# Optimization experiments

Measured on AMD Instinct MI355X. Metric: run time of the kernel, lower is better.

## Reference

```python
import jax, jax.numpy as jnp
import numpy as np

B, N, H, D = 8, 2048, 8, 64  # batch, seq, heads, head_dim
DM = H * D                   # model dim = 512


def setup_inputs() -> dict:
    key = jax.random.key(0)
    ks = jax.random.split(key, 9)
    std = 0.02
    return {
        "x": jax.random.normal(ks[0], (B, N, DM), dtype=jnp.float32),
        "Wq": jax.random.normal(ks[1], (H, D, D), dtype=jnp.float32) * std,
        "bq": jnp.zeros((H, D), dtype=jnp.float32),
        "Wk": jax.random.normal(ks[2], (H, D, D), dtype=jnp.float32) * std,
        "bk": jnp.zeros((H, D), dtype=jnp.float32),
        "Wv": jax.random.normal(ks[3], (H, D, D), dtype=jnp.float32) * std,
        "bv": jnp.zeros((H, D), dtype=jnp.float32),
        "Wp": jax.random.normal(ks[4], (DM, DM), dtype=jnp.float32) * std,
        "bp": jnp.zeros((DM,), dtype=jnp.float32),
    }


def reference(x, Wq, bq, Wk, bk, Wv, bv, Wp, bp):
    b, n, dm = x.shape
    # rearrange 'b n (h d) -> b h n d'
    xh = x.reshape(b, n, H, D).transpose(0, 2, 1, 3)  # [b,h,n,d]
    # per-head linear projections (torch Linear: y = x W^T + b), batched over heads
    q = jnp.einsum('bhnd,hed->bhne', xh, Wq) + bq[None, :, None, :]
    k = jnp.einsum('bhnd,hed->bhne', xh, Wk) + bk[None, :, None, :]
    v = jnp.einsum('bhnd,hed->bhne', xh, Wv) + bv[None, :, None, :]
    scale = 1.0 / jnp.sqrt(jnp.asarray(D, dtype=x.dtype))
    scores = jnp.einsum('bhqe,bhke->bhqk', q, k) * scale  # [b,h,n,n]
    attn = jax.nn.softmax(scores, axis=-1)
    out = jnp.einsum('bhqk,bhke->bhqe', attn, v)          # [b,h,n,d]
    # 'b h n d -> b n (h d)' then output projection
    out = out.transpose(0, 2, 1, 3).reshape(b, n, H * D)
    return out @ Wp.T + bp
```

## Files before the change

### kernel.cpp

```cpp
#include <hip/hip_runtime.h>
#include <hip/hip_bf16.h>

#define B_ 8
#define N_ 2048
#define H_ 8
#define DM_ 512
#define NT_ 32

typedef __bf16 bf16x8 __attribute__((ext_vector_type(8)));
typedef float f32x4 __attribute__((ext_vector_type(4)));
typedef float f32x16 __attribute__((ext_vector_type(16)));
typedef unsigned short us8 __attribute__((ext_vector_type(8)));
typedef unsigned short us4 __attribute__((ext_vector_type(4)));
typedef unsigned int u32x4 __attribute__((ext_vector_type(4)));

#define QSCALE 0.1803368801111204f

__device__ __forceinline__ int swz(int row, int byte_in_row) {
  return row * 128 + (byte_in_row ^ ((row & 7) << 4));
}

__device__ __forceinline__ unsigned short f2bf(float x) {
  __bf16 h = (__bf16)x;
  return __builtin_bit_cast(unsigned short, h);
}

__device__ __forceinline__ float fexp2(float x) {
#if __has_builtin(__builtin_amdgcn_exp2f)
  return __builtin_amdgcn_exp2f(x);
#else
  return exp2f(x);
#endif
}

__device__ __forceinline__ unsigned cvtpk(float a, float b) {
  unsigned r;
  asm("v_cvt_pk_bf16_f32 %0, %1, %2" : "=v"(r) : "v"(a), "v"(b));
  return r;
}

__device__ __forceinline__ f32x4 mfma16(bf16x8 a, bf16x8 b, f32x4 c) {
  return __builtin_amdgcn_mfma_f32_16x16x32_bf16(a, b, c, 0, 0, 0);
}
__device__ __forceinline__ f32x16 mfma32(bf16x8 a, bf16x8 b, f32x16 c) {
  return __builtin_amdgcn_mfma_f32_32x32x16_bf16(a, b, c, 0, 0, 0);
}

__device__ __forceinline__ bf16x8 ldg8(const unsigned short* p) {
  return *reinterpret_cast<const bf16x8*>(p);
}

__device__ __forceinline__ void stage_f32_tile(const float* __restrict__ src,
                                               int src_stride, char* dst, int t) {
#pragma unroll
  for (int rep = 0; rep < 4; ++rep) {
    int cid = rep * 256 + t;
    int row = cid >> 4, c4 = cid & 15;
    float4 v = *reinterpret_cast<const float4*>(src + (size_t)row * src_stride + c4 * 4);
    us4 o;
    o[0] = f2bf(v.x); o[1] = f2bf(v.y); o[2] = f2bf(v.z); o[3] = f2bf(v.w);
    *reinterpret_cast<us4*>(dst + row * 128 + ((c4 * 8) ^ ((row & 7) << 4))) = o;
  }
}

__device__ __forceinline__ void stage_bf16_tile(const unsigned short* __restrict__ src,
                                                int src_stride, char* dst, int t) {
#pragma unroll
  for (int rep = 0; rep < 2; ++rep) {
    int cid = rep * 256 + t;
    int row = cid >> 3, c = cid & 7;
    us8 v = *reinterpret_cast<const us8*>(src + (size_t)row * src_stride + c * 8);
    *reinterpret_cast<us8*>(dst + row * 128 + ((c * 16) ^ ((row & 7) << 4))) = v;
  }
}

__global__ __launch_bounds__(256, 4) void qkv_kernel(
    const float* __restrict__ x,
    const float* __restrict__ Wq, const float* __restrict__ bq,
    const float* __restrict__ Wk, const float* __restrict__ bk,
    const float* __restrict__ Wv, const float* __restrict__ bv,
    unsigned short* __restrict__ Qf, unsigned short* __restrict__ Kf,
    unsigned short* __restrict__ Vf) {
  __shared__ __align__(16) char sX[8192];
  __shared__ __align__(16) char sWq[8192];
  __shared__ __align__(16) char sWk[8192];
  __shared__ __align__(16) char sWv[8192];

  const int t = threadIdx.x;
  const int bh = blockIdx.y, h = bh & 7, b = bh >> 3;
  const int n0 = blockIdx.x * 64;
  const int lane = t & 63, w = t >> 6, g = lane >> 4, li = lane & 15;

  stage_f32_tile(x + ((size_t)(b * N_ + n0)) * DM_ + h * 64, DM_, sX, t);
  stage_f32_tile(Wq + (size_t)h * 4096, 64, sWq, t);
  stage_f32_tile(Wk + (size_t)h * 4096, 64, sWk, t);
  stage_f32_tile(Wv + (size_t)h * 4096, 64, sWv, t);
  __syncthreads();

  bf16x8 xa0 = *reinterpret_cast<const bf16x8*>(sX + swz(16 * w + li, 16 * g));
  bf16x8 xa1 = *reinterpret_cast<const bf16x8*>(sX + swz(16 * w + li, 64 + 16 * g));

  const size_t seg = (size_t)N_ * 64;
  const int qkbase =
      ((n0 >> 5) + (w >> 1)) * 2048 + (li >> 3) * 256 + (w & 1) * 128 + (li & 7);
  const int vbase =
      (n0 >> 6) * 4096 + w * 512 + (g >> 1) * 256 + 4 * (g & 1) + li * 8;

  unsigned short* Qs = Qf + (size_t)bh * seg;
  unsigned short* Ks = Kf + (size_t)bh * seg;
  unsigned short* Vs = Vf + (size_t)bh * seg;

#pragma unroll
  for (int c = 0; c < 4; ++c) {
    f32x4 a = {0.f, 0.f, 0.f, 0.f};
    bf16x8 b0 = *reinterpret_cast<const bf16x8*>(sWq + swz(c * 16 + li, 16 * g));
    bf16x8 b1 = *reinterpret_cast<const bf16x8*>(sWq + swz(c * 16 + li, 64 + 16 * g));
    a = mfma16(xa0, b0, a);
    a = mfma16(xa1, b1, a);
    float bb = bq[h * 64 + c * 16 + li];
#pragma unroll
    for (int i = 0; i < 4; ++i)
      Qs[qkbase + c * 512 + (4 * g + i) * 8] = f2bf((a[i] + bb) * QSCALE);
  }
#pragma unroll
  for (int c = 0; c < 4; ++c) {
    f32x4 a = {0.f, 0.f, 0.f, 0.f};
    bf16x8 b0 = *reinterpret_cast<const bf16x8*>(sWk + swz(c * 16 + li, 16 * g));
    bf16x8 b1 = *reinterpret_cast<const bf16x8*>(sWk + swz(c * 16 + li, 64 + 16 * g));
    a = mfma16(xa0, b0, a);
    a = mfma16(xa1, b1, a);
    float bb = bk[h * 64 + c * 16 + li];
#pragma unroll
    for (int i = 0; i < 4; ++i)
      Ks[qkbase + c * 512 + (4 * g + i) * 8] = f2bf(a[i] + bb);
  }
#pragma unroll
  for (int c = 0; c < 4; ++c) {
    f32x4 a = {0.f, 0.f, 0.f, 0.f};
    bf16x8 b0 = *reinterpret_cast<const bf16x8*>(sWv + swz(c * 16 + li, 16 * g));
    bf16x8 b1 = *reinterpret_cast<const bf16x8*>(sWv + swz(c * 16 + li, 64 + 16 * g));
    a = mfma16(xa0, b0, a);
    a = mfma16(xa1, b1, a);
    float bb = bv[h * 64 + c * 16 + li];
    us4 pk;
#pragma unroll
    for (int i = 0; i < 4; ++i) pk[i] = f2bf(a[i] + bb);
    *reinterpret_cast<us4*>(Vs + vbase + (c >> 1) * 2048 + (c & 1) * 128) = pk;
  }
}

__global__ __launch_bounds__(256, 3) void attn_kernel(
    const unsigned short* __restrict__ Qf, const unsigned short* __restrict__ Kf,
    const unsigned short* __restrict__ Vf, unsigned short* __restrict__ AOw) {
  const int t = threadIdx.x;
  const int lane = t & 63, w = t >> 6;
  const int lo = lane & 31, hi = lane >> 5;
  const bool hb = hi != 0;

  const int bid = blockIdx.x;
  const int work = (bid & 7) * 128 + (bid >> 3);
  const int bh = work >> 4;
  const int qb = (work & 15) * 4 + w;
  const int h = bh & 7, b = bh >> 3;

  const size_t seg = (size_t)N_ * 64;
  const unsigned short* qp = Qf + (size_t)bh * seg + qb * 2048 + lane * 8;
  const unsigned short* kp = Kf + (size_t)bh * seg + lane * 8;
  const unsigned short* vp = Vf + (size_t)bh * seg + lane * 8;

  bf16x8 qf[4];
#pragma unroll
  for (int dd = 0; dd < 4; ++dd) qf[dd] = ldg8(qp + dd * 512);

  f32x16 o0 = {}, o1 = {};
  float m = -__builtin_inff(), l = 0.f;

#pragma unroll 1
  for (int kt = 0; kt < NT_; ++kt) {
    const unsigned short* kpt = kp + kt * 4096;
    const unsigned short* vpt = vp + kt * 4096;
    bf16x8 kf0[4], kf1[4], vf0[4], vf1[4];
#pragma unroll
    for (int dd = 0; dd < 4; ++dd) {
      kf0[dd] = ldg8(kpt + dd * 512);
      kf1[dd] = ldg8(kpt + 2048 + dd * 512);
    }
#pragma unroll
    for (int ks = 0; ks < 4; ++ks) {
      vf0[ks] = ldg8(vpt + ks * 512);
      vf1[ks] = ldg8(vpt + 2048 + ks * 512);
    }

    f32x16 s0 = {}, s1 = {};
    __builtin_amdgcn_s_setprio(1);
#pragma unroll
    for (int dd = 0; dd < 4; ++dd) {
      s0 = mfma32(kf0[dd], qf[dd], s0);
      s1 = mfma32(kf1[dd], qf[dd], s1);
    }
    __builtin_amdgcn_s_setprio(0);

    float pm;
    {
      float a0 = fmaxf(s0[0], s0[1]), a1 = fmaxf(s0[2], s0[3]);
      float a2 = fmaxf(s0[4], s0[5]), a3 = fmaxf(s0[6], s0[7]);
      float a4 = fmaxf(s0[8], s0[9]), a5 = fmaxf(s0[10], s0[11]);
      float a6 = fmaxf(s0[12], s0[13]), a7 = fmaxf(s0[14], s0[15]);
      float b0 = fmaxf(s1[0], s1[1]), b1 = fmaxf(s1[2], s1[3]);
      float b2 = fmaxf(s1[4], s1[5]), b3 = fmaxf(s1[6], s1[7]);
      float b4 = fmaxf(s1[8], s1[9]), b5 = fmaxf(s1[10], s1[11]);
      float b6 = fmaxf(s1[12], s1[13]), b7 = fmaxf(s1[14], s1[15]);
      a0 = fmaxf(fmaxf(a0, a1), fmaxf(a2, a3));
      a4 = fmaxf(fmaxf(a4, a5), fmaxf(a6, a7));
      b0 = fmaxf(fmaxf(b0, b1), fmaxf(b2, b3));
      b4 = fmaxf(fmaxf(b4, b5), fmaxf(b6, b7));
      pm = fmaxf(fmaxf(a0, a4), fmaxf(b0, b4));
    }
    pm = fmaxf(pm, __shfl_xor(pm, 32));

    if (!__all(pm <= m + 8.0f)) {
      float mn = fmaxf(m, pm);
      float al = fexp2(m - mn);
      l *= al;
#pragma unroll
      for (int r = 0; r < 16; ++r) { o0[r] *= al; o1[r] *= al; }
      m = mn;
    }

    float ts0 = 0.f, ts1 = 0.f, ts2 = 0.f, ts3 = 0.f;
#pragma unroll
    for (int r = 0; r < 16; r += 4) {
      s0[r + 0] = fexp2(s0[r + 0] - m); ts0 += s0[r + 0];
      s0[r + 1] = fexp2(s0[r + 1] - m); ts1 += s0[r + 1];
      s0[r + 2] = fexp2(s0[r + 2] - m); ts2 += s0[r + 2];
      s0[r + 3] = fexp2(s0[r + 3] - m); ts3 += s0[r + 3];
      s1[r + 0] = fexp2(s1[r + 0] - m); ts0 += s1[r + 0];
      s1[r + 1] = fexp2(s1[r + 1] - m); ts1 += s1[r + 1];
      s1[r + 2] = fexp2(s1[r + 2] - m); ts2 += s1[r + 2];
      s1[r + 3] = fexp2(s1[r + 3] - m); ts3 += s1[r + 3];
    }
    float ts = (ts0 + ts1) + (ts2 + ts3);
    ts += __shfl_xor(ts, 32);
    l += ts;

    unsigned pl0[4], ph0[4], pl1[4], ph1[4];
#pragma unroll
    for (int qi = 0; qi < 4; ++qi) {
      pl0[qi] = cvtpk(s0[4 * qi + 0], s0[4 * qi + 1]);
      ph0[qi] = cvtpk(s0[4 * qi + 2], s0[4 * qi + 3]);
      pl1[qi] = cvtpk(s1[4 * qi + 0], s1[4 * qi + 1]);
      ph1[qi] = cvtpk(s1[4 * qi + 2], s1[4 * qi + 3]);
    }
    bf16x8 pf[4];
#pragma unroll
    for (int ks = 0; ks < 4; ++ks) {
      const int p = ks & 1;
      unsigned k0l, k0h, k1l, k1h;
      if (ks < 2) { k0l = pl0[2 * p]; k0h = ph0[2 * p]; k1l = pl0[2 * p + 1]; k1h = ph0[2 * p + 1]; }
      else        { k0l = pl1[2 * p]; k0h = ph1[2 * p]; k1l = pl1[2 * p + 1]; k1h = ph1[2 * p + 1]; }
      unsigned sl = hb ? k0l : k1l, sh = hb ? k0h : k1h;
      unsigned rl = __shfl_xor(sl, 32), rh = __shfl_xor(sh, 32);
      unsigned Al = hb ? rl : k0l, Ah = hb ? rh : k0h;
      unsigned Bl = hb ? k1l : rl, Bh = hb ? k1h : rh;
      u32x4 words = {Al, Ah, Bl, Bh};
      pf[ks] = __builtin_bit_cast(bf16x8, words);
    }

    __builtin_amdgcn_s_setprio(1);
#pragma unroll
    for (int ks = 0; ks < 4; ++ks) {
      o0 = mfma32(vf0[ks], pf[ks], o0);
      o1 = mfma32(vf1[ks], pf[ks], o1);
    }
    __builtin_amdgcn_s_setprio(0);
  }

  const float invl = 1.0f / l;
  unsigned short* aoptr =
      AOw + ((size_t)(b * N_) + qb * 32 + lo) * DM_ + h * 64 + 4 * hi;
#pragma unroll
  for (int qi = 0; qi < 4; ++qi) {
    us4 pk;
#pragma unroll
    for (int rr = 0; rr < 4; ++rr) pk[rr] = f2bf(o0[4 * qi + rr] * invl);
    *reinterpret_cast<us4*>(aoptr + 8 * qi) = pk;
  }
#pragma unroll
  for (int qi = 0; qi < 4; ++qi) {
    us4 pk;
#pragma unroll
    for (int rr = 0; rr < 4; ++rr) pk[rr] = f2bf(o1[4 * qi + rr] * invl);
    *reinterpret_cast<us4*>(aoptr + 32 + 8 * qi) = pk;
  }
}

__global__ __launch_bounds__(256, 4) void proj_kernel(
    const unsigned short* __restrict__ AOw, const float* __restrict__ Wp,
    const float* __restrict__ bp, float* __restrict__ out) {
  __shared__ __align__(16) char sA[8192];
  __shared__ __align__(16) char sB[8192];

  const int t = threadIdx.x;
  const int r0 = blockIdx.x * 64;
  const int i0 = blockIdx.y * 64;
  const int lane = t & 63, w = t >> 6, g = lane >> 4, li = lane & 15;

  f32x4 acc[4];
#pragma unroll
  for (int c = 0; c < 4; ++c) {
    acc[c][0] = 0.f; acc[c][1] = 0.f; acc[c][2] = 0.f; acc[c][3] = 0.f;
  }

  for (int jt = 0; jt < 8; ++jt) {
    __syncthreads();
    stage_bf16_tile(AOw + (size_t)r0 * DM_ + jt * 64, DM_, sA, t);
    stage_f32_tile(Wp + (size_t)i0 * DM_ + jt * 64, DM_, sB, t);
    __syncthreads();

    bf16x8 a0 = *reinterpret_cast<const bf16x8*>(sA + swz(16 * w + li, 16 * g));
    bf16x8 a1 = *reinterpret_cast<const bf16x8*>(sA + swz(16 * w + li, 64 + 16 * g));
#pragma unroll
    for (int c = 0; c < 4; ++c) {
      bf16x8 b0 = *reinterpret_cast<const bf16x8*>(sB + swz(c * 16 + li, 16 * g));
      bf16x8 b1 = *reinterpret_cast<const bf16x8*>(sB + swz(c * 16 + li, 64 + 16 * g));
      acc[c] = mfma16(a0, b0, acc[c]);
      acc[c] = mfma16(a1, b1, acc[c]);
    }
  }

#pragma unroll
  for (int c = 0; c < 4; ++c) {
    float bb = bp[i0 + c * 16 + li];
#pragma unroll
    for (int i = 0; i < 4; ++i)
      out[(size_t)(r0 + 16 * w + 4 * g + i) * DM_ + i0 + c * 16 + li] = acc[c][i] + bb;
  }
}

extern "C" void kernel_launch(void* const* d_in, const int* in_sizes, int n_in,
                              void* d_out, int out_size, void* d_ws, size_t ws_size,
                              hipStream_t stream) {
  const float* x  = (const float*)d_in[0];
  const float* Wq = (const float*)d_in[1];
  const float* bq = (const float*)d_in[2];
  const float* Wk = (const float*)d_in[3];
  const float* bk = (const float*)d_in[4];
  const float* Wv = (const float*)d_in[5];
  const float* bv = (const float*)d_in[6];
  const float* Wp = (const float*)d_in[7];
  const float* bp = (const float*)d_in[8];
  float* out = (float*)d_out;

  const size_t seg = (size_t)B_ * H_ * N_ * 64;
  unsigned short* Qf  = (unsigned short*)d_ws;
  unsigned short* Kf  = Qf + seg;
  unsigned short* Vf  = Kf + seg;
  unsigned short* AOw = Vf + seg;

  qkv_kernel<<<dim3(32, 64), 256, 0, stream>>>(x, Wq, bq, Wk, bk, Wv, bv, Qf, Kf, Vf);
  attn_kernel<<<dim3(1024), 256, 0, stream>>>(Qf, Kf, Vf, AOw);
  proj_kernel<<<dim3(256, 8), 256, 0, stream>>>(AOw, Wp, bp, out);
}
```

Measured before the change: 148.4 us.

## Prefetch next K tile, fold max subtraction into MFMA init, use permlane32 swap

The attention inner loop is unrolled by two with ping-pong K register buffers, so the next tile's K fragments load while the current tile computes. The running max is subtracted by seeding the score accumulators with -m, which drops the per-element subtraction before exp2. The shfl_xor plus select sequence that exchanges P halves across lanes is replaced with v_permlane32_swap. The double K buffer adds register pressure, which could hurt occupancy under launch_bounds(256,3).

```diff
diff --git a/kernel.cpp b/kernel.cpp
--- a/kernel.cpp
+++ b/kernel.cpp
@@ -37,6 +37,16 @@
   unsigned r;
   asm("v_cvt_pk_bf16_f32 %0, %1, %2" : "=v"(r) : "v"(a), "v"(b));
   return r;
+}
+
+__device__ __forceinline__ void plswap(unsigned& a, unsigned& b) {
+#if __has_builtin(__builtin_amdgcn_permlane32_swap)
+  auto r = __builtin_amdgcn_permlane32_swap(a, b, false, false);
+  a = r[0];
+  b = r[1];
+#else
+  asm("v_permlane32_swap_b32 %0, %1" : "+v"(a), "+v"(b));
+#endif
 }
 
 __device__ __forceinline__ f32x4 mfma16(bf16x8 a, bf16x8 b, f32x4 c) {
@@ -154,8 +164,7 @@
     const unsigned short* __restrict__ Vf, unsigned short* __restrict__ AOw) {
   const int t = threadIdx.x;
   const int lane = t & 63, w = t >> 6;
-  const int lo = lane & 31, hi = lane >> 5;
-  const bool hb = hi != 0;
+  const int lo = lane & 31;
 
   const int bid = blockIdx.x;
   const int work = (bid & 7) * 128 + (bid >> 3);
@@ -172,31 +181,34 @@
 #pragma unroll
   for (int dd = 0; dd < 4; ++dd) qf[dd] = ldg8(qp + dd * 512);
 
+  bf16x8 kA[8], kB[8];
+#pragma unroll
+  for (int j = 0; j < 8; ++j) kA[j] = ldg8(kp + j * 512);
+
   f32x16 o0 = {}, o1 = {};
-  float m = -__builtin_inff(), l = 0.f;
-
-#pragma unroll 1
-  for (int kt = 0; kt < NT_; ++kt) {
-    const unsigned short* kpt = kp + kt * 4096;
-    const unsigned short* vpt = vp + kt * 4096;
-    bf16x8 kf0[4], kf1[4], vf0[4], vf1[4];
+  float m = 0.f, l = 0.f;
+
+  auto TILE = [&](int kt, bf16x8(&kC)[8], bf16x8(&kN)[8]) {
+    bf16x8 vf[8];
+    const unsigned short* vpt = vp + (size_t)kt * 4096;
+#pragma unroll
+    for (int j = 0; j < 8; ++j) vf[j] = ldg8(vpt + j * 512);
+    if (kt + 1 < NT_) {
+      const unsigned short* kpt = kp + (size_t)(kt + 1) * 4096;
+#pragma unroll
+      for (int j = 0; j < 8; ++j) kN[j] = ldg8(kpt + j * 512);
+    }
+
+    const float nm = -m;
+    f32x16 s0, s1;
+#pragma unroll
+    for (int r = 0; r < 16; ++r) { s0[r] = nm; s1[r] = nm; }
+
+    __builtin_amdgcn_s_setprio(1);
 #pragma unroll
     for (int dd = 0; dd < 4; ++dd) {
-      kf0[dd] = ldg8(kpt + dd * 512);
-      kf1[dd] = ldg8(kpt + 2048 + dd * 512);
-    }
-#pragma unroll
-    for (int ks = 0; ks < 4; ++ks) {
-      vf0[ks] = ldg8(vpt + ks * 512);
-      vf1[ks] = ldg8(vpt + 2048 + ks * 512);
-    }
-
-    f32x16 s0 = {}, s1 = {};
-    __builtin_amdgcn_s_setprio(1);
-#pragma unroll
-    for (int dd = 0; dd < 4; ++dd) {
-      s0 = mfma32(kf0[dd], qf[dd], s0);
-      s1 = mfma32(kf1[dd], qf[dd], s1);
+      s0 = mfma32(kC[dd], qf[dd], s0);
+      s1 = mfma32(kC[4 + dd], qf[dd], s1);
     }
     __builtin_amdgcn_s_setprio(0);
 
@@ -218,26 +230,29 @@
     }
     pm = fmaxf(pm, __shfl_xor(pm, 32));
 
-    if (!__all(pm <= m + 8.0f)) {
-      float mn = fmaxf(m, pm);
-      float al = fexp2(m - mn);
+    if (!__all(pm <= 8.0f)) {
+      float d = fmaxf(pm, 0.0f);
+      float al = fexp2(-d);
       l *= al;
 #pragma unroll
-      for (int r = 0; r < 16; ++r) { o0[r] *= al; o1[r] *= al; }
-      m = mn;
+      for (int r = 0; r < 16; ++r) {
+        o0[r] *= al; o1[r] *= al;
+        s0[r] -= d; s1[r] -= d;
+      }
+      m += d;
     }
 
     float ts0 = 0.f, ts1 = 0.f, ts2 = 0.f, ts3 = 0.f;
 #pragma unroll
     for (int r = 0; r < 16; r += 4) {
-      s0[r + 0] = fexp2(s0[r + 0] - m); ts0 += s0[r + 0];
-      s0[r + 1] = fexp2(s0[r + 1] - m); ts1 += s0[r + 1];
-      s0[r + 2] = fexp2(s0[r + 2] - m); ts2 += s0[r + 2];
-      s0[r + 3] = fexp2(s0[r + 3] - m); ts3 += s0[r + 3];
-      s1[r + 0] = fexp2(s1[r + 0] - m); ts0 += s1[r + 0];
-      s1[r + 1] = fexp2(s1[r + 1] - m); ts1 += s1[r + 1];
-      s1[r + 2] = fexp2(s1[r + 2] - m); ts2 += s1[r + 2];
-      s1[r + 3] = fexp2(s1[r + 3] - m); ts3 += s1[r + 3];
+      s0[r + 0] = fexp2(s0[r + 0]); ts0 += s0[r + 0];
+      s0[r + 1] = fexp2(s0[r + 1]); ts1 += s0[r + 1];
+      s0[r + 2] = fexp2(s0[r + 2]); ts2 += s0[r + 2];
+      s0[r + 3] = fexp2(s0[r + 3]); ts3 += s0[r + 3];
+      s1[r + 0] = fexp2(s1[r + 0]); ts0 += s1[r + 0];
+      s1[r + 1] = fexp2(s1[r + 1]); ts1 += s1[r + 1];
+      s1[r + 2] = fexp2(s1[r + 2]); ts2 += s1[r + 2];
+      s1[r + 3] = fexp2(s1[r + 3]); ts3 += s1[r + 3];
     }
     float ts = (ts0 + ts1) + (ts2 + ts3);
     ts += __shfl_xor(ts, 32);
@@ -251,30 +266,38 @@
       pl1[qi] = cvtpk(s1[4 * qi + 0], s1[4 * qi + 1]);
       ph1[qi] = cvtpk(s1[4 * qi + 2], s1[4 * qi + 3]);
     }
+    plswap(pl0[0], pl0[1]); plswap(ph0[0], ph0[1]);
+    plswap(pl0[2], pl0[3]); plswap(ph0[2], ph0[3]);
+    plswap(pl1[0], pl1[1]); plswap(ph1[0], ph1[1]);
+    plswap(pl1[2], pl1[3]); plswap(ph1[2], ph1[3]);
     bf16x8 pf[4];
+    {
+      u32x4 w0 = {pl0[0], ph0[0], pl0[1], ph0[1]};
+      u32x4 w1 = {pl0[2], ph0[2], pl0[3], ph0[3]};
+      u32x4 w2 = {pl1[0], ph1[0], pl1[1], ph1[1]};
+      u32x4 w3 = {pl1[2], ph1[2], pl1[3], ph1[3]};
+      pf[0] = __builtin_bit_cast(bf16x8, w0);
+      pf[1] = __builtin_bit_cast(bf16x8, w1);
+      pf[2] = __builtin_bit_cast(bf16x8, w2);
+      pf[3] = __builtin_bit_cast(bf16x8, w3);
+    }
+
+    __builtin_amdgcn_s_setprio(1);
 #pragma unroll
     for (int ks = 0; ks < 4; ++ks) {
-      const int p = ks & 1;
-      unsigned k0l, k0h, k1l, k1h;
-      if (ks < 2) { k0l = pl0[2 * p]; k0h = ph0[2 * p]; k1l = pl0[2 * p + 1]; k1h = ph0[2 * p + 1]; }
-      else        { k0l = pl1[2 * p]; k0h = ph1[2 * p]; k1l = pl1[2 * p + 1]; k1h = ph1[2 * p + 1]; }
-      unsigned sl = hb ? k0l : k1l, sh = hb ? k0h : k1h;
-      unsigned rl = __shfl_xor(sl, 32), rh = __shfl_xor(sh, 32);
-      unsigned Al = hb ? rl : k0l, Ah = hb ? rh : k0h;
-      unsigned Bl = hb ? k1l : rl, Bh = hb ? k1h : rh;
-      u32x4 words = {Al, Ah, Bl, Bh};
-      pf[ks] = __builtin_bit_cast(bf16x8, words);
-    }
-
-    __builtin_amdgcn_s_setprio(1);
-#pragma unroll
-    for (int ks = 0; ks < 4; ++ks) {
-      o0 = mfma32(vf0[ks], pf[ks], o0);
-      o1 = mfma32(vf1[ks], pf[ks], o1);
+      o0 = mfma32(vf[ks], pf[ks], o0);
+      o1 = mfma32(vf[4 + ks], pf[ks], o1);
     }
     __builtin_amdgcn_s_setprio(0);
-  }
-
+  };
+
+#pragma unroll 1
+  for (int kt2 = 0; kt2 < NT_ / 2; ++kt2) {
+    TILE(2 * kt2, kA, kB);
+    TILE(2 * kt2 + 1, kB, kA);
+  }
+
+  const int hi = lane >> 5;
   const float invl = 1.0f / l;
   unsigned short* aoptr =
       AOw + ((size_t)(b * N_) + qb * 32 + lo) * DM_ + h * 64 + 4 * hi;
```

Measured after the change: 236.1 us. +59.1%, slower.
